# Kernel tuning notes

Hardware: AMD Instinct MI355X
Metric: run time of the kernel (lower is better)

Reference implementation:

```python
import jax, jax.numpy as jnp
import numpy as np

K = 3
PAD = 1
EPS = 1e-5


def _unfold(x, k, pad):
    # torch.nn.Unfold(k, dilation=1, padding=pad, stride=1): output [B, C*k*k, L]
    # with channel-major ordering (c, ki, kj) in the second dim.
    B, C, H, W = x.shape
    xp = jnp.pad(x, ((0, 0), (0, 0), (pad, pad), (pad, pad)))
    Ho = H + 2 * pad - k + 1
    Wo = W + 2 * pad - k + 1
    patches = jnp.stack(
        [xp[:, :, i:i + Ho, j:j + Wo] for i in range(k) for j in range(k)],
        axis=2,
    )  # [B, C, k*k, Ho, Wo]
    return patches.reshape(B, C * k * k, Ho * Wo)


def _conv1x1(x, w, b):
    return jnp.einsum('bchw,oc->bohw', x, w) + b[None, :, None, None]


def _bn(x, g, b):
    # training-mode BatchNorm2d: batch stats over (B,H,W), biased variance
    mu = x.mean(axis=(0, 2, 3), keepdims=True)
    var = x.var(axis=(0, 2, 3), keepdims=True)
    return (x - mu) * jax.lax.rsqrt(var + EPS) * g[None, :, None, None] + b[None, :, None, None]


def _tri(x, w, b, g, be):
    return jax.nn.relu(_bn(_conv1x1(x, w, b), g, be))


def reference(x, w1, b1, g1, be1, w2, b2, g2, be2, wf, bf, gf, bef):
    B, C, H, W = x.shape
    k2 = K * K
    c = k2 // 2
    tri1 = _tri(x, w1, b1, g1, be1)  # key map  [B,C,H,W] (m=1)
    tri2 = _tri(x, w2, b2, g2, be2)  # query map
    # NOTE: faithful to source: plain row-major reshape of [B, C*k2, L] -> [B, C, L, k2]
    ku = _unfold(tri1, K, PAD).reshape(B, C, -1, k2)
    qu = _unfold(tri2, K, PAD).reshape(B, C, -1, k2)
    logits = ku * qu[..., c:c + 1] + ku[..., c:c + 1] * qu
    dl_weight = jax.nn.softmax(logits, axis=-1)[:, None]  # [B,1,C,L,k2]
    xu = _unfold(x, K, PAD).reshape(B, 1, C, -1, k2)       # m=1 -> [B,1,C,L,k2]
    # NOTE: faithful to source: row-major reshape to [B, C, k2, L], sum over axis -2
    pre = (dl_weight * xu).reshape(B, C, k2, -1).sum(axis=-2).reshape(B, C, H, W)
    return jax.nn.relu(_bn(_conv1x1(pre, wf, bf), gf, bef))


def setup_inputs() -> dict:
    key = jax.random.key(0)
    B, C, O, H, W = 4, 256, 256, 64, 64
    ks = jax.random.split(key, 4)
    s = 1.0 / np.sqrt(C)
    return {
        'x': jax.random.normal(ks[0], (B, C, H, W), dtype=jnp.float32),
        'w1': jax.random.normal(ks[1], (C, C), dtype=jnp.float32) * s,
        'b1': jnp.zeros((C,), jnp.float32),
        'g1': jnp.ones((C,), jnp.float32),
        'be1': jnp.zeros((C,), jnp.float32),
        'w2': jax.random.normal(ks[2], (C, C), dtype=jnp.float32) * s,
        'b2': jnp.zeros((C,), jnp.float32),
        'g2': jnp.ones((C,), jnp.float32),
        'be2': jnp.zeros((C,), jnp.float32),
        'wf': jax.random.normal(ks[3], (O, C), dtype=jnp.float32) * s,
        'bf': jnp.zeros((O,), jnp.float32),
        'gf': jnp.ones((O,), jnp.float32),
        'bef': jnp.zeros((O,), jnp.float32),
    }
```

## Files before the change

### kernel.cpp

```cpp
#include <hip/hip_runtime.h>
#include <hip/hip_bf16.h>

#define L 4096
#define CCH 256
#define NB 4
#define KP 40
#define GOF 72
#define LOG2E 1.4426950408889634f

typedef __attribute__((ext_vector_type(8))) short short8;
typedef __attribute__((ext_vector_type(4))) float f32x4;
typedef unsigned short ushort_t;

__device__ __forceinline__ unsigned short f2bf(float f) {
    unsigned u = __builtin_bit_cast(unsigned, f);
    u += 0x7FFF + ((u >> 16) & 1);
    return (unsigned short)(u >> 16);
}
__device__ __forceinline__ unsigned pk_bf16(float a, float b) {
    __hip_bfloat162 h = __float22bfloat162_rn(make_float2(a, b));
    unsigned u;
    __builtin_memcpy(&u, &h, 4);
    return u;
}
__device__ __forceinline__ float bflo(unsigned w) {
    return __builtin_bit_cast(float, w << 16);
}
__device__ __forceinline__ float bfhi(unsigned w) {
    return __builtin_bit_cast(float, w & 0xFFFF0000u);
}
__device__ __forceinline__ float bfu(ushort_t h) {
    return __builtin_bit_cast(float, (unsigned)h << 16);
}

__global__ __launch_bounds__(256) void wcvt_k(
    const float* __restrict__ w1, const float* __restrict__ w2,
    const float* __restrict__ wf,
    ushort_t* __restrict__ wb1, ushort_t* __restrict__ wb2,
    ushort_t* __restrict__ wbf)
{
    const int mb = blockIdx.x >> 6;
    const int i  = (blockIdx.x & 63) * 256 + threadIdx.x;
    const float* src = (mb == 0) ? w1 : (mb == 1) ? w2 : wf;
    ushort_t*    dst = (mb == 0) ? wb1 : (mb == 1) ? wb2 : wbf;
    float4 v = ((const float4*)src)[i];
    uint2 p;
    p.x = pk_bf16(v.x, v.y);
    p.y = pk_bf16(v.z, v.w);
    ((uint2*)dst)[i] = p;
}

__global__ __launch_bounds__(256, 3) void dual_gemm_k(
    const float* __restrict__ x,
    const ushort_t* __restrict__ wb1, const float* __restrict__ b1,
    const ushort_t* __restrict__ wb2, const float* __restrict__ b2,
    ushort_t* __restrict__ y1, ushort_t* __restrict__ y2)
{
    __shared__ short sA1[2][128 * KP];
    __shared__ short sA2[2][128 * KP];
    __shared__ short sB [2][64 * KP];

    const int tid = threadIdx.x;
    const int l0 = blockIdx.x * 64;
    const int o0 = blockIdx.y * 128;
    const int b  = blockIdx.z;

    const int wv = tid >> 6;
    const int lane = tid & 63;
    const int m = lane & 15;
    const int quad = lane >> 4;

    const float* xb = x + (size_t)b * CCH * L;

    const int sl = tid & 63, soct = tid >> 6;
    const int sr = tid & 127, sh = tid >> 7;

    f32x4 acc1[2][4], acc2[2][4];
    #pragma unroll
    for (int io = 0; io < 2; ++io)
        #pragma unroll
        for (int jl = 0; jl < 4; ++jl) {
            acc1[io][jl] = (f32x4){0.f,0.f,0.f,0.f};
            acc2[io][jl] = (f32x4){0.f,0.f,0.f,0.f};
        }

    float fx[8];
    uint4 pw1a, pw1b, pw2a, pw2b;

    auto LOADT = [&](int s) {
        const int k0 = s * 32;
        const float* xs = xb + (size_t)(k0 + soct * 8) * L + l0 + sl;
        #pragma unroll
        for (int j = 0; j < 8; ++j) fx[j] = xs[(size_t)j * L];
        const uint4* wp = (const uint4*)&wb1[(size_t)(o0 + sr) * CCH + k0 + sh * 16];
        pw1a = wp[0]; pw1b = wp[1];
        const uint4* wq = (const uint4*)&wb2[(size_t)(o0 + sr) * CCH + k0 + sh * 16];
        pw2a = wq[0]; pw2b = wq[1];
    };
    auto STORET = [&](int buf) {
        uint4 v;
        v.x = pk_bf16(fx[0], fx[1]);
        v.y = pk_bf16(fx[2], fx[3]);
        v.z = pk_bf16(fx[4], fx[5]);
        v.w = pk_bf16(fx[6], fx[7]);
        *(uint4*)&sB[buf][sl * KP + soct * 8] = v;
        *(uint4*)&sA1[buf][sr * KP + sh * 16]     = pw1a;
        *(uint4*)&sA1[buf][sr * KP + sh * 16 + 8] = pw1b;
        *(uint4*)&sA2[buf][sr * KP + sh * 16]     = pw2a;
        *(uint4*)&sA2[buf][sr * KP + sh * 16 + 8] = pw2b;
    };

    LOADT(0);
    STORET(0);
    __syncthreads();

    for (int s = 0; s < 8; ++s) {
        const int buf = s & 1;
        if (s < 7) LOADT(s + 1);

        short8 a1[2], a2[2], bfr[4];
        #pragma unroll
        for (int io = 0; io < 2; ++io) {
            a1[io] = *(const short8*)&sA1[buf][(wv * 32 + io * 16 + m) * KP + quad * 8];
            a2[io] = *(const short8*)&sA2[buf][(wv * 32 + io * 16 + m) * KP + quad * 8];
        }
        #pragma unroll
        for (int jl = 0; jl < 4; ++jl)
            bfr[jl] = *(const short8*)&sB[buf][(jl * 16 + m) * KP + quad * 8];
        #pragma unroll
        for (int io = 0; io < 2; ++io)
            #pragma unroll
            for (int jl = 0; jl < 4; ++jl) {
                acc1[io][jl] = __builtin_amdgcn_mfma_f32_16x16x32_bf16(a1[io], bfr[jl], acc1[io][jl], 0, 0, 0);
                acc2[io][jl] = __builtin_amdgcn_mfma_f32_16x16x32_bf16(a2[io], bfr[jl], acc2[io][jl], 0, 0, 0);
            }

        if (s < 7) STORET(buf ^ 1);
        __syncthreads();
    }

    #pragma unroll
    for (int io = 0; io < 2; ++io)
        #pragma unroll
        for (int reg = 0; reg < 4; ++reg) {
            const int o = o0 + wv * 32 + io * 16 + quad * 4 + reg;
            const float bb1 = b1[o], bb2 = b2[o];
            const size_t ro = ((size_t)b * CCH + o) * L + l0 + m;
            unsigned u1a = pk_bf16(acc1[io][0][reg] + bb1, acc1[io][1][reg] + bb1);
            unsigned u1b = pk_bf16(acc1[io][2][reg] + bb1, acc1[io][3][reg] + bb1);
            unsigned u2a = pk_bf16(acc2[io][0][reg] + bb2, acc2[io][1][reg] + bb2);
            unsigned u2b = pk_bf16(acc2[io][2][reg] + bb2, acc2[io][3][reg] + bb2);
            y1[ro]      = (ushort_t)u1a;
            y1[ro + 16] = (ushort_t)(u1a >> 16);
            y1[ro + 32] = (ushort_t)u1b;
            y1[ro + 48] = (ushort_t)(u1b >> 16);
            y2[ro]      = (ushort_t)u2a;
            y2[ro + 16] = (ushort_t)(u2a >> 16);
            y2[ro + 32] = (ushort_t)u2b;
            y2[ro + 48] = (ushort_t)(u2b >> 16);
        }
}

__global__ __launch_bounds__(256, 4) void single_gemm_k(
    const ushort_t* __restrict__ x,
    const ushort_t* __restrict__ wb, const float* __restrict__ bb,
    ushort_t* __restrict__ y)
{
    __shared__ short sA[2][128 * KP];
    __shared__ short sB[2][64 * KP];

    const int tid = threadIdx.x;
    const int l0 = blockIdx.x * 64;
    const int o0 = blockIdx.y * 128;
    const int b  = blockIdx.z;

    const int wv = tid >> 6;
    const int lane = tid & 63;
    const int m = lane & 15;
    const int quad = lane >> 4;

    const ushort_t* xb = x + (size_t)b * CCH * L;

    const int sl = tid & 63, soct = tid >> 6;
    const int sr = tid & 127, sh = tid >> 7;

    f32x4 acc[2][4];
    #pragma unroll
    for (int io = 0; io < 2; ++io)
        #pragma unroll
        for (int jl = 0; jl < 4; ++jl)
            acc[io][jl] = (f32x4){0.f,0.f,0.f,0.f};

    ushort_t hx[8];
    uint4 pwa, pwb;

    auto LOADT = [&](int s) {
        const int k0 = s * 32;
        const ushort_t* xs = xb + (size_t)(k0 + soct * 8) * L + l0 + sl;
        #pragma unroll
        for (int j = 0; j < 8; ++j) hx[j] = xs[(size_t)j * L];
        const uint4* wp = (const uint4*)&wb[(size_t)(o0 + sr) * CCH + k0 + sh * 16];
        pwa = wp[0]; pwb = wp[1];
    };
    auto STORET = [&](int buf) {
        short8 v;
        #pragma unroll
        for (int j = 0; j < 8; ++j) v[j] = (short)hx[j];
        *(short8*)&sB[buf][sl * KP + soct * 8] = v;
        *(uint4*)&sA[buf][sr * KP + sh * 16]     = pwa;
        *(uint4*)&sA[buf][sr * KP + sh * 16 + 8] = pwb;
    };

    LOADT(0);
    STORET(0);
    __syncthreads();

    for (int s = 0; s < 8; ++s) {
        const int buf = s & 1;
        if (s < 7) LOADT(s + 1);

        short8 a[2], bfr[4];
        #pragma unroll
        for (int io = 0; io < 2; ++io)
            a[io] = *(const short8*)&sA[buf][(wv * 32 + io * 16 + m) * KP + quad * 8];
        #pragma unroll
        for (int jl = 0; jl < 4; ++jl)
            bfr[jl] = *(const short8*)&sB[buf][(jl * 16 + m) * KP + quad * 8];
        #pragma unroll
        for (int io = 0; io < 2; ++io)
            #pragma unroll
            for (int jl = 0; jl < 4; ++jl)
                acc[io][jl] = __builtin_amdgcn_mfma_f32_16x16x32_bf16(a[io], bfr[jl], acc[io][jl], 0, 0, 0);

        if (s < 7) STORET(buf ^ 1);
        __syncthreads();
    }

    #pragma unroll
    for (int io = 0; io < 2; ++io)
        #pragma unroll
        for (int reg = 0; reg < 4; ++reg) {
            const int o = o0 + wv * 32 + io * 16 + quad * 4 + reg;
            const float b0 = bb[o];
            const size_t ro = ((size_t)b * CCH + o) * L + l0 + m;
            unsigned ua = pk_bf16(acc[io][0][reg] + b0, acc[io][1][reg] + b0);
            unsigned ub = pk_bf16(acc[io][2][reg] + b0, acc[io][3][reg] + b0);
            y[ro]      = (ushort_t)ua;
            y[ro + 16] = (ushort_t)(ua >> 16);
            y[ro + 32] = (ushort_t)ub;
            y[ro + 48] = (ushort_t)(ub >> 16);
        }
}

__device__ __forceinline__ void bn_stats_body(
    const ushort_t* y, const float* gamma, const float* beta,
    float* scale, float* shift, int c, int tid, float kscale)
{
    float s = 0.f, s2 = 0.f;
    for (int b = 0; b < NB; ++b) {
        const uint4* p = (const uint4*)(y + ((size_t)b * CCH + c) * L);
        #pragma unroll
        for (int r = 0; r < 2; ++r) {
            uint4 v = p[r * 256 + tid];
            unsigned w[4] = {v.x, v.y, v.z, v.w};
            #pragma unroll
            for (int u = 0; u < 4; ++u) {
                float a = bflo(w[u]), bb = bfhi(w[u]);
                s  += a + bb;
                s2 += a * a + bb * bb;
            }
        }
    }
    #pragma unroll
    for (int off = 32; off > 0; off >>= 1) {
        s  += __shfl_down(s, off);
        s2 += __shfl_down(s2, off);
    }
    __shared__ float red[2][4];
    if ((tid & 63) == 0) { red[0][tid >> 6] = s; red[1][tid >> 6] = s2; }
    __syncthreads();
    if (tid == 0) {
        float S  = red[0][0] + red[0][1] + red[0][2] + red[0][3];
        float S2 = red[1][0] + red[1][1] + red[1][2] + red[1][3];
        const float invN = 1.f / (NB * (float)L);
        float mean = S * invN;
        float var  = S2 * invN - mean * mean;
        float rstd = rsqrtf(var + 1e-5f);
        float g = gamma[c];
        scale[c] = kscale * g * rstd;
        shift[c] = kscale * (beta[c] - mean * g * rstd);
    }
}

__global__ __launch_bounds__(256) void bn_stats2_k(
    const ushort_t* __restrict__ y1, const float* __restrict__ g1, const float* __restrict__ be1,
    float* __restrict__ sc1, float* __restrict__ sh1,
    const ushort_t* __restrict__ y2, const float* __restrict__ g2, const float* __restrict__ be2,
    float* __restrict__ sc2, float* __restrict__ sh2)
{
    const int c = blockIdx.x & 255;
    if (blockIdx.x < 256) bn_stats_body(y1, g1, be1, sc1, sh1, c, threadIdx.x, LOG2E);
    else                  bn_stats_body(y2, g2, be2, sc2, sh2, c, threadIdx.x, 1.0f);
}

__global__ __launch_bounds__(512, 6) void attention_k(
    const float* __restrict__ x,
    const ushort_t* __restrict__ y1,
    const ushort_t* __restrict__ y2,
    const float* __restrict__ s1sc, const float* __restrict__ s1sh,
    const float* __restrict__ s2sc, const float* __restrict__ s2sh,
    ushort_t* __restrict__ pre)
{
    __shared__ unsigned sKQg[4240];
    __shared__ ushort_t sXg [4240];
    __shared__ float    accF[L];

    const int bc = blockIdx.x;
    const int tid = threadIdx.x;
    const int ch = bc & 255;
    const size_t off = (size_t)bc * L;

    const float sc1 = s1sc[ch], sh1 = s1sh[ch];
    const float sc2 = s2sc[ch], sh2 = s2sh[ch];

    if (tid < GOF)  { sKQg[tid] = 0; sXg[tid] = 0; }
    if (tid < 72)   { sKQg[GOF + 4096 + tid] = 0; sXg[GOF + 4096 + tid] = 0; }
    {
        float4 z = {0.f, 0.f, 0.f, 0.f};
        ((float4*)accF)[tid]       = z;
        ((float4*)accF)[tid + 512] = z;
    }
    {
        uint4 ak = ((const uint4*)(y1 + off))[tid];
        uint4 aq = ((const uint4*)(y2 + off))[tid];
        float4 xa = ((const float4*)(x + off))[2 * tid];
        float4 xb = ((const float4*)(x + off))[2 * tid + 1];
        unsigned wk[4] = {ak.x, ak.y, ak.z, ak.w};
        unsigned wq[4] = {aq.x, aq.y, aq.z, aq.w};
        unsigned kq[8];
        #pragma unroll
        for (int u = 0; u < 4; ++u) {
            float klo = fmaxf(fmaf(bflo(wk[u]), sc1, sh1), 0.f);
            float khi = fmaxf(fmaf(bfhi(wk[u]), sc1, sh1), 0.f);
            float qlo = fmaxf(fmaf(bflo(wq[u]), sc2, sh2), 0.f);
            float qhi = fmaxf(fmaf(bfhi(wq[u]), sc2, sh2), 0.f);
            kq[2*u]   = (unsigned)f2bf(klo) | ((unsigned)f2bf(qlo) << 16);
            kq[2*u+1] = (unsigned)f2bf(khi) | ((unsigned)f2bf(qhi) << 16);
        }
        *(uint4*)&sKQg[GOF + 8 * tid]     = make_uint4(kq[0], kq[1], kq[2], kq[3]);
        *(uint4*)&sKQg[GOF + 8 * tid + 4] = make_uint4(kq[4], kq[5], kq[6], kq[7]);
        float xv[8] = {xa.x, xa.y, xa.z, xa.w, xb.x, xb.y, xb.z, xb.w};
        unsigned xp[4];
        #pragma unroll
        for (int u = 0; u < 4; ++u)
            xp[u] = (unsigned)f2bf(xv[2*u]) | ((unsigned)f2bf(xv[2*u+1]) << 16);
        *(uint4*)&sXg[GOF + 8 * tid] = make_uint4(xp[0], xp[1], xp[2], xp[3]);
    }
    __syncthreads();

    {
        const int fbase = 9 * tid;
        #pragma unroll
        for (int r = 0; r < 8; ++r) {
            const int f  = fbase + 4608 * r;
            const int t  = f >> 12;
            const int fl = f & 4095;
            unsigned wv[9];
            float    xw[9];
            const bool fastp = (fl < 4088);
            if (fastp) {
                const int di = (t * 86) >> 8;
                const int dj = t - 3 * di;
                const int cbad = (dj == 0) ? 0 : ((dj == 2) ? 63 : 99);
                const int base = fl + (di << 6) + dj - 65 + GOF;
                #pragma unroll
                for (int j = 0; j < 9; ++j) {
                    wv[j] = sKQg[base + j];
                    xw[j] = bfu(sXg[base + j]);
                }
                #pragma unroll
                for (int j = 0; j < 9; ++j) {
                    int c = (fl + j) & 63;
                    bool bad = (c == cbad);
                    wv[j] = bad ? 0u  : wv[j];
                    xw[j] = bad ? 0.f : xw[j];
                }
            } else {
                #pragma unroll
                for (int j = 0; j < 9; ++j) {
                    int fj = f + j;
                    int tj = fj >> 12, lj = fj & 4095;
                    int dij = (tj * 86) >> 8, djj = tj - 3 * dij;
                    int idx = lj + (dij << 6) + djj - 65 + GOF;
                    unsigned wr = sKQg[idx];
                    float    xr = bfu(sXg[idx]);
                    int c = lj & 63;
                    int cb = (djj == 0) ? 0 : ((djj == 2) ? 63 : 99);
                    bool bad = (c == cb);
                    wv[j] = bad ? 0u  : wr;
                    xw[j] = bad ? 0.f : xr;
                }
            }
            const unsigned cw = wv[4];
            const float kc = bflo(cw), qc = bfhi(cw);
            float e[9];
            #pragma unroll
            for (int j = 0; j < 9; ++j)
                e[j] = __builtin_amdgcn_exp2f(bflo(wv[j]) * qc + kc * bfhi(wv[j]));
            float s = (((e[0] + e[1]) + (e[2] + e[3])) +
                       ((e[4] + e[5]) + (e[6] + e[7]))) + e[8];
            const float rinv = __builtin_amdgcn_rcpf(s);
            float cj[9];
            #pragma unroll
            for (int j = 0; j < 9; ++j)
                cj[j] = e[j] * rinv * xw[j];

            __syncthreads();
            if (tid < 455) {
                if (fastp) {
                    #pragma unroll
                    for (int j = 0; j < 9; ++j) accF[fl + j] += cj[j];
                } else {
                    #pragma unroll
                    for (int j = 0; j < 9; ++j) accF[(f + j) & 4095] += cj[j];
                }
            }
            __syncthreads();
            if (tid >= 455) {
                if (fastp) {
                    #pragma unroll
                    for (int j = 0; j < 9; ++j) accF[fl + j] += cj[j];
                } else {
                    #pragma unroll
                    for (int j = 0; j < 9; ++j) accF[(f + j) & 4095] += cj[j];
                }
            }
        }
    }
    __syncthreads();

    {
        unsigned* po = (unsigned*)(pre + off);
        #pragma unroll
        for (int rr = 0; rr < 4; ++rr) {
            const int p = rr * 512 + tid;
            po[p] = pk_bf16(accF[2 * p], accF[2 * p + 1]);
        }
    }
}

__global__ __launch_bounds__(256) void bn_fused_k(
    const ushort_t* __restrict__ yf,
    const float* __restrict__ gf, const float* __restrict__ bef,
    float* __restrict__ out)
{
    __shared__ uint4 sY[2048];
    __shared__ float red[2][4];
    __shared__ float fsc, fsh;

    const int c = blockIdx.x, tid = threadIdx.x;
    float s = 0.f, s2 = 0.f;
    #pragma unroll
    for (int b = 0; b < NB; ++b) {
        const uint4* p = (const uint4*)(yf + ((size_t)b * CCH + c) * L);
        #pragma unroll
        for (int r = 0; r < 2; ++r) {
            uint4 v = p[r * 256 + tid];
            sY[b * 512 + r * 256 + tid] = v;
            unsigned w[4] = {v.x, v.y, v.z, v.w};
            #pragma unroll
            for (int u = 0; u < 4; ++u) {
                float a = bflo(w[u]), bb = bfhi(w[u]);
                s  += a + bb;
                s2 += a * a + bb * bb;
            }
        }
    }
    #pragma unroll
    for (int off = 32; off > 0; off >>= 1) {
        s  += __shfl_down(s, off);
        s2 += __shfl_down(s2, off);
    }
    if ((tid & 63) == 0) { red[0][tid >> 6] = s; red[1][tid >> 6] = s2; }
    __syncthreads();
    if (tid == 0) {
        float S  = red[0][0] + red[0][1] + red[0][2] + red[0][3];
        float S2 = red[1][0] + red[1][1] + red[1][2] + red[1][3];
        const float invN = 1.f / (NB * (float)L);
        float mean = S * invN;
        float var  = S2 * invN - mean * mean;
        float rstd = rsqrtf(var + 1e-5f);
        float g = gf[c];
        fsc = g * rstd;
        fsh = bef[c] - mean * g * rstd;
    }
    __syncthreads();
    const float sc = fsc, sh = fsh;

    #pragma unroll
    for (int b = 0; b < NB; ++b) {
        float4* o = (float4*)(out + ((size_t)b * CCH + c) * L);
        #pragma unroll
        for (int r = 0; r < 2; ++r) {
            uint4 v = sY[b * 512 + r * 256 + tid];
            unsigned w[4] = {v.x, v.y, v.z, v.w};
            float4 o0, o1;
            o0.x = fmaxf(fmaf(bflo(w[0]), sc, sh), 0.f);
            o0.y = fmaxf(fmaf(bfhi(w[0]), sc, sh), 0.f);
            o0.z = fmaxf(fmaf(bflo(w[1]), sc, sh), 0.f);
            o0.w = fmaxf(fmaf(bfhi(w[1]), sc, sh), 0.f);
            o1.x = fmaxf(fmaf(bflo(w[2]), sc, sh), 0.f);
            o1.y = fmaxf(fmaf(bfhi(w[2]), sc, sh), 0.f);
            o1.z = fmaxf(fmaf(bflo(w[3]), sc, sh), 0.f);
            o1.w = fmaxf(fmaf(bfhi(w[3]), sc, sh), 0.f);
            int i = r * 256 + tid;
            o[2 * i]     = o0;
            o[2 * i + 1] = o1;
        }
    }
}

extern "C" void kernel_launch(void* const* d_in, const int* in_sizes, int n_in,
                              void* d_out, int out_size, void* d_ws, size_t ws_size,
                              hipStream_t stream) {
    const float* x   = (const float*)d_in[0];
    const float* w1  = (const float*)d_in[1];
    const float* b1  = (const float*)d_in[2];
    const float* g1  = (const float*)d_in[3];
    const float* be1 = (const float*)d_in[4];
    const float* w2  = (const float*)d_in[5];
    const float* b2  = (const float*)d_in[6];
    const float* g2  = (const float*)d_in[7];
    const float* be2 = (const float*)d_in[8];
    const float* wf  = (const float*)d_in[9];
    const float* bf  = (const float*)d_in[10];
    const float* gf  = (const float*)d_in[11];
    const float* bef = (const float*)d_in[12];
    float* out = (float*)d_out;

    const size_t NEL = (size_t)NB * CCH * L;
    ushort_t* y1b = (ushort_t*)d_ws;
    ushort_t* y2b = y1b + NEL;
    float* st = (float*)(y2b + NEL);
    float* s1sc = st,        *s1sh = st + 256;
    float* s2sc = st + 512,  *s2sh = st + 768;
    ushort_t* wb1 = (ushort_t*)(st + 1536);
    ushort_t* wb2 = wb1 + CCH * CCH;
    ushort_t* wbf = wb2 + CCH * CCH;

    wcvt_k<<<192, 256, 0, stream>>>(w1, w2, wf, wb1, wb2, wbf);
    dim3 gg(64, 2, 4);
    dual_gemm_k<<<gg, 256, 0, stream>>>(x, wb1, b1, wb2, b2, y1b, y2b);
    bn_stats2_k<<<512, 256, 0, stream>>>(y1b, g1, be1, s1sc, s1sh,
                                         y2b, g2, be2, s2sc, s2sh);
    attention_k<<<NB * CCH, 512, 0, stream>>>(x, y1b, y2b,
                                              s1sc, s1sh, s2sc, s2sh,
                                              y2b);
    single_gemm_k<<<gg, 256, 0, stream>>>(y2b, wbf, bf, y1b);
    bn_fused_k<<<256, 256, 0, stream>>>(y1b, gf, bef, out);
}
```

Before: 160.7 us.

## Fuse BatchNorm statistics into GEMM epilogues via atomic per-channel accumulation

```diff
diff --git a/kernel.cpp b/kernel.cpp
--- a/kernel.cpp
+++ b/kernel.cpp
@@ -7,6 +7,7 @@
 #define KP 40
 #define GOF 72
 #define LOG2E 1.4426950408889634f
+#define INVN (1.0f / (NB * (float)L))
 
 typedef __attribute__((ext_vector_type(8))) short short8;
 typedef __attribute__((ext_vector_type(4))) float f32x4;
@@ -37,10 +38,14 @@
     const float* __restrict__ w1, const float* __restrict__ w2,
     const float* __restrict__ wf,
     ushort_t* __restrict__ wb1, ushort_t* __restrict__ wb2,
-    ushort_t* __restrict__ wbf)
+    ushort_t* __restrict__ wbf, float* __restrict__ st)
 {
     const int mb = blockIdx.x >> 6;
     const int i  = (blockIdx.x & 63) * 256 + threadIdx.x;
+    if (blockIdx.x == 0) {
+        #pragma unroll
+        for (int k = 0; k < 6; ++k) st[k * 256 + threadIdx.x] = 0.f;
+    }
     const float* src = (mb == 0) ? w1 : (mb == 1) ? w2 : wf;
     ushort_t*    dst = (mb == 0) ? wb1 : (mb == 1) ? wb2 : wbf;
     float4 v = ((const float4*)src)[i];
@@ -54,7 +59,9 @@
     const float* __restrict__ x,
     const ushort_t* __restrict__ wb1, const float* __restrict__ b1,
     const ushort_t* __restrict__ wb2, const float* __restrict__ b2,
-    ushort_t* __restrict__ y1, ushort_t* __restrict__ y2)
+    ushort_t* __restrict__ y1, ushort_t* __restrict__ y2,
+    float* __restrict__ stS1, float* __restrict__ stQ1,
+    float* __restrict__ stS2, float* __restrict__ stQ2)
 {
     __shared__ short sA1[2][128 * KP];
     __shared__ short sA2[2][128 * KP];
@@ -145,11 +152,17 @@
         for (int reg = 0; reg < 4; ++reg) {
             const int o = o0 + wv * 32 + io * 16 + quad * 4 + reg;
             const float bb1 = b1[o], bb2 = b2[o];
+            float v1[4], v2[4];
+            #pragma unroll
+            for (int jl = 0; jl < 4; ++jl) {
+                v1[jl] = acc1[io][jl][reg] + bb1;
+                v2[jl] = acc2[io][jl][reg] + bb2;
+            }
             const size_t ro = ((size_t)b * CCH + o) * L + l0 + m;
-            unsigned u1a = pk_bf16(acc1[io][0][reg] + bb1, acc1[io][1][reg] + bb1);
-            unsigned u1b = pk_bf16(acc1[io][2][reg] + bb1, acc1[io][3][reg] + bb1);
-            unsigned u2a = pk_bf16(acc2[io][0][reg] + bb2, acc2[io][1][reg] + bb2);
-            unsigned u2b = pk_bf16(acc2[io][2][reg] + bb2, acc2[io][3][reg] + bb2);
+            unsigned u1a = pk_bf16(v1[0], v1[1]);
+            unsigned u1b = pk_bf16(v1[2], v1[3]);
+            unsigned u2a = pk_bf16(v2[0], v2[1]);
+            unsigned u2b = pk_bf16(v2[2], v2[3]);
             y1[ro]      = (ushort_t)u1a;
             y1[ro + 16] = (ushort_t)(u1a >> 16);
             y1[ro + 32] = (ushort_t)u1b;
@@ -158,13 +171,28 @@
             y2[ro + 16] = (ushort_t)(u2a >> 16);
             y2[ro + 32] = (ushort_t)u2b;
             y2[ro + 48] = (ushort_t)(u2b >> 16);
+
+            float s1 = (v1[0] + v1[1]) + (v1[2] + v1[3]);
+            float q1 = (v1[0]*v1[0] + v1[1]*v1[1]) + (v1[2]*v1[2] + v1[3]*v1[3]);
+            float s2 = (v2[0] + v2[1]) + (v2[2] + v2[3]);
+            float q2 = (v2[0]*v2[0] + v2[1]*v2[1]) + (v2[2]*v2[2] + v2[3]*v2[3]);
+            #pragma unroll
+            for (int d = 1; d < 16; d <<= 1) {
+                s1 += __shfl_xor(s1, d); q1 += __shfl_xor(q1, d);
+                s2 += __shfl_xor(s2, d); q2 += __shfl_xor(q2, d);
+            }
+            if (m == 0) {
+                atomicAdd(&stS1[o], s1); atomicAdd(&stQ1[o], q1);
+                atomicAdd(&stS2[o], s2); atomicAdd(&stQ2[o], q2);
+            }
         }
 }
 
 __global__ __launch_bounds__(256, 4) void single_gemm_k(
     const ushort_t* __restrict__ x,
     const ushort_t* __restrict__ wb, const float* __restrict__ bb,
-    ushort_t* __restrict__ y)
+    ushort_t* __restrict__ y,
+    float* __restrict__ stS, float* __restrict__ stQ)
 {
     __shared__ short sA[2][128 * KP];
     __shared__ short sB[2][64 * KP];
@@ -242,73 +270,37 @@
         for (int reg = 0; reg < 4; ++reg) {
             const int o = o0 + wv * 32 + io * 16 + quad * 4 + reg;
             const float b0 = bb[o];
+            float v[4];
+            #pragma unroll
+            for (int jl = 0; jl < 4; ++jl) v[jl] = acc[io][jl][reg] + b0;
             const size_t ro = ((size_t)b * CCH + o) * L + l0 + m;
-            unsigned ua = pk_bf16(acc[io][0][reg] + b0, acc[io][1][reg] + b0);
-            unsigned ub = pk_bf16(acc[io][2][reg] + b0, acc[io][3][reg] + b0);
+            unsigned ua = pk_bf16(v[0], v[1]);
+            unsigned ub = pk_bf16(v[2], v[3]);
             y[ro]      = (ushort_t)ua;
             y[ro + 16] = (ushort_t)(ua >> 16);
             y[ro + 32] = (ushort_t)ub;
             y[ro + 48] = (ushort_t)(ub >> 16);
-        }
-}
-
-__device__ __forceinline__ void bn_stats_body(
-    const ushort_t* y, const float* gamma, const float* beta,
-    float* scale, float* shift, int c, int tid, float kscale)
-{
-    float s = 0.f, s2 = 0.f;
-    for (int b = 0; b < NB; ++b) {
-        const uint4* p = (const uint4*)(y + ((size_t)b * CCH + c) * L);
-        #pragma unroll
-        for (int r = 0; r < 2; ++r) {
-            uint4 v = p[r * 256 + tid];
-            unsigned w[4] = {v.x, v.y, v.z, v.w};
-            #pragma unroll
-            for (int u = 0; u < 4; ++u) {
-                float a = bflo(w[u]), bb = bfhi(w[u]);
-                s  += a + bb;
-                s2 += a * a + bb * bb;
-            }
-        }
-    }
-    #pragma unroll
-    for (int off = 32; off > 0; off >>= 1) {
-        s  += __shfl_down(s, off);
-        s2 += __shfl_down(s2, off);
-    }
-    __shared__ float red[2][4];
-    if ((tid & 63) == 0) { red[0][tid >> 6] = s; red[1][tid >> 6] = s2; }
-    __syncthreads();
-    if (tid == 0) {
-        float S  = red[0][0] + red[0][1] + red[0][2] + red[0][3];
-        float S2 = red[1][0] + red[1][1] + red[1][2] + red[1][3];
-        const float invN = 1.f / (NB * (float)L);
-        float mean = S * invN;
-        float var  = S2 * invN - mean * mean;
-        float rstd = rsqrtf(var + 1e-5f);
-        float g = gamma[c];
-        scale[c] = kscale * g * rstd;
-        shift[c] = kscale * (beta[c] - mean * g * rstd);
-    }
-}
-
-__global__ __launch_bounds__(256) void bn_stats2_k(
-    const ushort_t* __restrict__ y1, const float* __restrict__ g1, const float* __restrict__ be1,
-    float* __restrict__ sc1, float* __restrict__ sh1,
-    const ushort_t* __restrict__ y2, const float* __restrict__ g2, const float* __restrict__ be2,
-    float* __restrict__ sc2, float* __restrict__ sh2)
-{
-    const int c = blockIdx.x & 255;
-    if (blockIdx.x < 256) bn_stats_body(y1, g1, be1, sc1, sh1, c, threadIdx.x, LOG2E);
-    else                  bn_stats_body(y2, g2, be2, sc2, sh2, c, threadIdx.x, 1.0f);
+
+            float s0 = (v[0] + v[1]) + (v[2] + v[3]);
+            float q0 = (v[0]*v[0] + v[1]*v[1]) + (v[2]*v[2] + v[3]*v[3]);
+            #pragma unroll
+            for (int d = 1; d < 16; d <<= 1) {
+                s0 += __shfl_xor(s0, d); q0 += __shfl_xor(q0, d);
+            }
+            if (m == 0) {
+                atomicAdd(&stS[o], s0); atomicAdd(&stQ[o], q0);
+            }
+        }
 }
 
 __global__ __launch_bounds__(512, 6) void attention_k(
     const float* __restrict__ x,
     const ushort_t* __restrict__ y1,
     const ushort_t* __restrict__ y2,
-    const float* __restrict__ s1sc, const float* __restrict__ s1sh,
-    const float* __restrict__ s2sc, const float* __restrict__ s2sh,
+    const float* __restrict__ stS1, const float* __restrict__ stQ1,
+    const float* __restrict__ stS2, const float* __restrict__ stQ2,
+    const float* __restrict__ g1, const float* __restrict__ be1,
+    const float* __restrict__ g2, const float* __restrict__ be2,
     ushort_t* __restrict__ pre)
 {
     __shared__ unsigned sKQg[4240];
@@ -320,8 +312,21 @@
     const int ch = bc & 255;
     const size_t off = (size_t)bc * L;
 
-    const float sc1 = s1sc[ch], sh1 = s1sh[ch];
-    const float sc2 = s2sc[ch], sh2 = s2sh[ch];
+    float sc1, sh1, sc2, sh2;
+    {
+        float S = stS1[ch], Q = stQ1[ch];
+        float mean = S * INVN, var = Q * INVN - mean * mean;
+        float rstd = rsqrtf(var + 1e-5f);
+        float g = g1[ch];
+        sc1 = LOG2E * g * rstd;
+        sh1 = LOG2E * (be1[ch] - mean * g * rstd);
+        S = stS2[ch]; Q = stQ2[ch];
+        mean = S * INVN; var = Q * INVN - mean * mean;
+        rstd = rsqrtf(var + 1e-5f);
+        g = g2[ch];
+        sc2 = g * rstd;
+        sh2 = be2[ch] - mean * g * rstd;
+    }
 
     if (tid < GOF)  { sKQg[tid] = 0; sXg[tid] = 0; }
     if (tid < 72)   { sKQg[GOF + 4096 + tid] = 0; sXg[GOF + 4096 + tid] = 0; }
@@ -449,74 +454,41 @@
     }
 }
 
-__global__ __launch_bounds__(256) void bn_fused_k(
+__global__ __launch_bounds__(256) void bn_apply_k(
     const ushort_t* __restrict__ yf,
+    const float* __restrict__ stS, const float* __restrict__ stQ,
     const float* __restrict__ gf, const float* __restrict__ bef,
     float* __restrict__ out)
 {
-    __shared__ uint4 sY[2048];
-    __shared__ float red[2][4];
-    __shared__ float fsc, fsh;
-
-    const int c = blockIdx.x, tid = threadIdx.x;
-    float s = 0.f, s2 = 0.f;
+    const int c = blockIdx.x & 255;
+    const int b = blockIdx.x >> 8;
+    const int tid = threadIdx.x;
+
+    float S = stS[c], Q = stQ[c];
+    float mean = S * INVN, var = Q * INVN - mean * mean;
+    float rstd = rsqrtf(var + 1e-5f);
+    float g = gf[c];
+    const float sc = g * rstd;
+    const float sh = bef[c] - mean * g * rstd;
+
+    const uint4* p = (const uint4*)(yf + ((size_t)b * CCH + c) * L);
+    float4* o = (float4*)(out + ((size_t)b * CCH + c) * L);
     #pragma unroll
-    for (int b = 0; b < NB; ++b) {
-        const uint4* p = (const uint4*)(yf + ((size_t)b * CCH + c) * L);
-        #pragma unroll
-        for (int r = 0; r < 2; ++r) {
-            uint4 v = p[r * 256 + tid];
-            sY[b * 512 + r * 256 + tid] = v;
-            unsigned w[4] = {v.x, v.y, v.z, v.w};
-            #pragma unroll
-            for (int u = 0; u < 4; ++u) {
-                float a = bflo(w[u]), bb = bfhi(w[u]);
-                s  += a + bb;
-                s2 += a * a + bb * bb;
-            }
-        }
-    }
-    #pragma unroll
-    for (int off = 32; off > 0; off >>= 1) {
-        s  += __shfl_down(s, off);
-        s2 += __shfl_down(s2, off);
-    }
-    if ((tid & 63) == 0) { red[0][tid >> 6] = s; red[1][tid >> 6] = s2; }
-    __syncthreads();
-    if (tid == 0) {
-        float S  = red[0][0] + red[0][1] + red[0][2] + red[0][3];
-        float S2 = red[1][0] + red[1][1] + red[1][2] + red[1][3];
-        const float invN = 1.f / (NB * (float)L);
-        float mean = S * invN;
-        float var  = S2 * invN - mean * mean;
-        float rstd = rsqrtf(var + 1e-5f);
-        float g = gf[c];
-        fsc = g * rstd;
-        fsh = bef[c] - mean * g * rstd;
-    }
-    __syncthreads();
-    const float sc = fsc, sh = fsh;
-
-    #pragma unroll
-    for (int b = 0; b < NB; ++b) {
-        float4* o = (float4*)(out + ((size_t)b * CCH + c) * L);
-        #pragma unroll
-        for (int r = 0; r < 2; ++r) {
-            uint4 v = sY[b * 512 + r * 256 + tid];
-            unsigned w[4] = {v.x, v.y, v.z, v.w};
-            float4 o0, o1;
-            o0.x = fmaxf(fmaf(bflo(w[0]), sc, sh), 0.f);
-            o0.y = fmaxf(fmaf(bfhi(w[0]), sc, sh), 0.f);
-            o0.z = fmaxf(fmaf(bflo(w[1]), sc, sh), 0.f);
-            o0.w = fmaxf(fmaf(bfhi(w[1]), sc, sh), 0.f);
-            o1.x = fmaxf(fmaf(bflo(w[2]), sc, sh), 0.f);
-            o1.y = fmaxf(fmaf(bfhi(w[2]), sc, sh), 0.f);
-            o1.z = fmaxf(fmaf(bflo(w[3]), sc, sh), 0.f);
-            o1.w = fmaxf(fmaf(bfhi(w[3]), sc, sh), 0.f);
-            int i = r * 256 + tid;
-            o[2 * i]     = o0;
-            o[2 * i + 1] = o1;
-        }
+    for (int r = 0; r < 2; ++r) {
+        uint4 v = p[r * 256 + tid];
+        unsigned w[4] = {v.x, v.y, v.z, v.w};
+        float4 o0, o1;
+        o0.x = fmaxf(fmaf(bflo(w[0]), sc, sh), 0.f);
+        o0.y = fmaxf(fmaf(bfhi(w[0]), sc, sh), 0.f);
+        o0.z = fmaxf(fmaf(bflo(w[1]), sc, sh), 0.f);
+        o0.w = fmaxf(fmaf(bfhi(w[1]), sc, sh), 0.f);
+        o1.x = fmaxf(fmaf(bflo(w[2]), sc, sh), 0.f);
+        o1.y = fmaxf(fmaf(bfhi(w[2]), sc, sh), 0.f);
+        o1.z = fmaxf(fmaf(bflo(w[3]), sc, sh), 0.f);
+        o1.w = fmaxf(fmaf(bfhi(w[3]), sc, sh), 0.f);
+        int i = r * 256 + tid;
+        o[2 * i]     = o0;
+        o[2 * i + 1] = o1;
     }
 }
 
@@ -542,20 +514,22 @@
     ushort_t* y1b = (ushort_t*)d_ws;
     ushort_t* y2b = y1b + NEL;
     float* st = (float*)(y2b + NEL);
-    float* s1sc = st,        *s1sh = st + 256;
-    float* s2sc = st + 512,  *s2sh = st + 768;
+    float* stS1 = st,        *stQ1 = st + 256;
+    float* stS2 = st + 512,  *stQ2 = st + 768;
+    float* stSF = st + 1024, *stQF = st + 1280;
     ushort_t* wb1 = (ushort_t*)(st + 1536);
     ushort_t* wb2 = wb1 + CCH * CCH;
     ushort_t* wbf = wb2 + CCH * CCH;
 
-    wcvt_k<<<192, 256, 0, stream>>>(w1, w2, wf, wb1, wb2, wbf);
+    wcvt_k<<<192, 256, 0, stream>>>(w1, w2, wf, wb1, wb2, wbf, st);
     dim3 gg(64, 2, 4);
-    dual_gemm_k<<<gg, 256, 0, stream>>>(x, wb1, b1, wb2, b2, y1b, y2b);
-    bn_stats2_k<<<512, 256, 0, stream>>>(y1b, g1, be1, s1sc, s1sh,
-                                         y2b, g2, be2, s2sc, s2sh);
+    dual_gemm_k<<<gg, 256, 0, stream>>>(x, wb1, b1, wb2, b2, y1b, y2b,
+                                        stS1, stQ1, stS2, stQ2);
     attention_k<<<NB * CCH, 512, 0, stream>>>(x, y1b, y2b,
-                                              s1sc, s1sh, s2sc, s2sh,
+                                              stS1, stQ1, stS2, stQ2,
+                                              g1, be1, g2, be2,
                                               y2b);
-    single_gemm_k<<<gg, 256, 0, stream>>>(y2b, wbf, bf, y1b);
-    bn_fused_k<<<256, 256, 0, stream>>>(y1b, gf, bef, out);
-}
+    single_gemm_k<<<gg, 256, 0, stream>>>(y2b, wbf, bf, y1b,
+                                          stSF, stQF);
+    bn_apply_k<<<NB * CCH, 256, 0, stream>>>(y1b, stSF, stQF, gf, bef, out);
+}
```

Result: slower. 202.3 us (+25.9%).
